# Performance work log

Measured on AMD Instinct MI355X. Metric: run time of the kernel, lower is better.

Reference implementation:

```python
import jax, jax.numpy as jnp
import numpy as np

EPS = 1e-6
BIG = 1e10

# ---- exact Euclidean distance transform (same math as the O(HW*Nfg) brute force,
# factored over rows: d^2(p, fg) = min_{r'} [ (y-r')^2 + min_{x': fg[r',x']} (x-x')^2 ] ----
def edt_2d(fg):  # fg: [H, W] bool -> [H, W] float distance to nearest True pixel
    H, W = fg.shape
    x = jnp.arange(W, dtype=jnp.float32)
    col_d2 = (x[:, None] - x[None, :]) ** 2                              # [W(x), W(x')]
    # colmin[r', x] = min over fg columns x' in row r' of (x-x')^2
    colmin = jnp.min(jnp.where(fg[:, None, :], col_d2[None, :, :], BIG), axis=-1)  # [H, W]
    y = jnp.arange(H, dtype=jnp.float32)
    row_d2 = (y[:, None] - y[None, :]) ** 2                              # [H(y), H(r')]
    d2 = jnp.min(colmin[None, :, :] + row_d2[:, :, None], axis=1)        # [H, W]
    max_dist = jnp.sqrt(jnp.asarray((H - 1) ** 2 + (W - 1) ** 2, jnp.float32))
    has_fg = jnp.any(fg)
    d2_safe = jnp.minimum(d2, (max_dist ** 2))  # only hit when fg empty
    return jnp.where(has_fg, jnp.sqrt(d2_safe), max_dist)


def signed_distance_map(gt):  # gt: [B,1,H,W] float in {0,1}
    gt_bool = gt[:, 0] > 0.5                                             # [B,H,W]
    dist_outside = jax.vmap(edt_2d)(gt_bool)
    dist_inside = jax.vmap(edt_2d)(~gt_bool)
    phi = jnp.where(gt_bool, -dist_inside, dist_outside)                 # [B,H,W]
    return phi[:, None]                                                  # [B,1,H,W]


def boundary_loss(s_theta, g):
    phi = signed_distance_map(g)
    weight = jnp.exp(-jnp.abs(phi) / 10.0)
    return jnp.mean(weight * jnp.abs(phi * s_theta))


def bce_loss(p, t):  # torch nn.BCELoss (log clamped at -100)
    logp = jnp.clip(jnp.log(p), -100.0)
    log1mp = jnp.clip(jnp.log(1.0 - p), -100.0)
    return -jnp.mean(t * logp + (1.0 - t) * log1mp)


def focal_loss(pred, target, alpha=0.25, gamma=2.0):
    pred = jnp.clip(pred, EPS, 1.0 - EPS)
    pt = pred * target + (1.0 - pred) * (1.0 - target)
    alpha_t = alpha * target + (1.0 - alpha) * (1.0 - target)
    return jnp.mean(-alpha_t * (1.0 - pt) ** gamma * jnp.log(pt))


def _gaussian_kernel(ksize=11, sigma=1.5):
    c = (ksize - 1) / 2.0
    g = np.exp(-((np.arange(ksize) - c) ** 2) / (2.0 * sigma ** 2))
    g = g / g.sum()
    k = np.outer(g, g).astype(np.float32)
    return jnp.asarray(k)[None, None]  # [1,1,K,K]

_SSIM_K = _gaussian_kernel()


def _gconv(x):  # x: [B,1,H,W], valid gaussian filter
    return jax.lax.conv_general_dilated(x, _SSIM_K, (1, 1), 'VALID',
                                        dimension_numbers=('NCHW', 'OIHW', 'NCHW'))


def ssim(x, y, data_range=1.0):
    C1 = (0.01 * data_range) ** 2
    C2 = (0.03 * data_range) ** 2
    mu_x, mu_y = _gconv(x), _gconv(y)
    sx = _gconv(x * x) - mu_x ** 2
    sy = _gconv(y * y) - mu_y ** 2
    sxy = _gconv(x * y) - mu_x * mu_y
    num = (2 * mu_x * mu_y + C1) * (2 * sxy + C2)
    den = (mu_x ** 2 + mu_y ** 2 + C1) * (sx + sy + C2)
    return jnp.mean(num / den)


DICE_W = 1.0
BOUNDARY_W = 1.0
FOCAL_W = 1.0
MSE_W = 1.0
FOCAL_ALPHA = 0.25
FOCAL_GAMMA = 2.0


def setup_inputs() -> dict:
    key = jax.random.key(0)
    k1, k2 = jax.random.split(key)
    pred_masks = jax.random.normal(k1, (8, 1, 192, 192), dtype=jnp.float32)
    target_masks = jax.random.randint(k2, (8, 1, 192, 192), 0, 2, dtype=jnp.int32)
    return {"pred_masks": pred_masks, "target_masks": target_masks}


def reference(pred_masks, target_masks):
    t = target_masks.astype(jnp.float32)
    p = jax.nn.sigmoid(pred_masks)
    dice_val = bce_loss(p, t) * DICE_W
    boundary_val = boundary_loss(p, t) * BOUNDARY_W
    focal_val = focal_loss(p, t, FOCAL_ALPHA, FOCAL_GAMMA) * FOCAL_W
    mse_val = ssim(p, t, 1.0) * MSE_W
    return dice_val + boundary_val + focal_val + mse_val
```

## Files before the change

### kernel.cpp

```cpp
#include <hip/hip_runtime.h>
#include <math.h>

#define BATCH 8
#define HH 192
#define WW 192
#define BIGF 1e10f
#define OH (HH - 10)
#define OW (WW - 10)
#define SSIM_ROWS 4
#define SSIM_BPI ((OH + SSIM_ROWS - 1) / SSIM_ROWS)
#define NSSIMBLK (BATCH * SSIM_BPI)
#define NMASKBLK (BATCH * HH)
#define NENVBLK (BATCH * WW)

__device__ __forceinline__ float waveReduceAdd(float v) {
    #pragma unroll
    for (int o = 32; o > 0; o >>= 1) v += __shfl_down(v, o, 64);
    return v;
}

__device__ __forceinline__ int nearestDist(const unsigned long long m0,
                                           const unsigned long long m1,
                                           const unsigned long long m2,
                                           int x) {
    const unsigned long long m[3] = {m0, m1, m2};
    const int wi = x >> 6, b = x & 63;
    int dL = 1 << 29;
    const unsigned long long low = m[wi] << (63 - b);
    if (low) dL = __clzll(low);
    else if (wi >= 1 && m[wi - 1]) dL = b + 1 + __clzll(m[wi - 1]);
    else if (wi == 2 && m[0]) dL = b + 65 + __clzll(m[0]);
    int dR = 1 << 29;
    const unsigned long long high = m[wi] >> b;
    if (high) dR = __ffsll((long long)high) - 1;
    else if (wi <= 1 && m[wi + 1]) dR = (64 - b) + __ffsll((long long)m[wi + 1]) - 1;
    else if (wi == 0 && m[2]) dR = (128 - b) + __ffsll((long long)m[2]) - 1;
    return min(dL, dR);
}

__global__ void prepKernel(const float* __restrict__ pred,
                           const int* __restrict__ tgt,
                           unsigned long long* __restrict__ mask,
                           float* __restrict__ ssimPart) {
    const int x = threadIdx.x;

    if (blockIdx.x >= NSSIMBLK) {
        const int blk = blockIdx.x - NSSIMBLK;
        const int b = blk / HH, r = blk % HH;
        const int t = tgt[(b * HH + r) * WW + x];
        const unsigned long long bal = __ballot(t > 0);
        if ((x & 63) == 0) mask[((size_t)b * 3 + (x >> 6)) * HH + r] = bal;
        return;
    }

    __shared__ __align__(16) float smem[SSIM_ROWS * 5 * WW];
    __shared__ float red1[3];
    const int blk = blockIdx.x;
    const int b = blk / SSIM_BPI;
    const int r0 = (blk % SSIM_BPI) * SSIM_ROWS;

    float g[11];
    {
        float s = 0.0f;
        #pragma unroll
        for (int k = 0; k < 11; ++k) {
            const float d = (float)(k - 5);
            g[k] = __expf(-d * d / 4.5f);
            s += g[k];
        }
        const float inv = 1.0f / s;
        #pragma unroll
        for (int k = 0; k < 11; ++k) g[k] *= inv;
    }

    float acc[SSIM_ROWS][5];
    #pragma unroll
    for (int o = 0; o < SSIM_ROWS; ++o)
        #pragma unroll
        for (int s = 0; s < 5; ++s) acc[o][s] = 0.0f;

    #pragma unroll
    for (int j = 0; j < SSIM_ROWS + 10; ++j) {
        const int row = r0 + j;
        float p = 0.0f, t = 0.0f;
        if (row < HH) {
            const float z = pred[(b * HH + row) * WW + x];
            p = 1.0f / (1.0f + __expf(-z));
            t = (float)tgt[(b * HH + row) * WW + x];
        }
        const float pp = p * p, tt = t * t, pt = p * t;
        #pragma unroll
        for (int o = 0; o < SSIM_ROWS; ++o) {
            const int k = j - o;
            if (k >= 0 && k <= 10) {
                const float gk = g[k];
                acc[o][0] += gk * p;  acc[o][1] += gk * t;
                acc[o][2] += gk * pp; acc[o][3] += gk * tt; acc[o][4] += gk * pt;
            }
        }
    }
    #pragma unroll
    for (int o = 0; o < SSIM_ROWS; ++o)
        #pragma unroll
        for (int s = 0; s < 5; ++s) smem[(o * 5 + s) * WW + x] = acc[o][s];
    __syncthreads();

    float term = 0.0f;
    if (x < OW) {
        #pragma unroll
        for (int o = 0; o < SSIM_ROWS; ++o) {
            if (r0 + o < OH) {
                float mx = 0, my = 0, mxx = 0, myy = 0, mxy = 0;
                #pragma unroll
                for (int k = 0; k < 11; ++k) {
                    mx  += g[k] * smem[(o * 5 + 0) * WW + x + k];
                    my  += g[k] * smem[(o * 5 + 1) * WW + x + k];
                    mxx += g[k] * smem[(o * 5 + 2) * WW + x + k];
                    myy += g[k] * smem[(o * 5 + 3) * WW + x + k];
                    mxy += g[k] * smem[(o * 5 + 4) * WW + x + k];
                }
                const float C1 = 1e-4f, C2 = 9e-4f;
                const float sx = mxx - mx * mx, sy = myy - my * my, sxy = mxy - mx * my;
                const float num = (2.0f * mx * my + C1) * (2.0f * sxy + C2);
                const float den = (mx * mx + my * my + C1) * (sx + sy + C2);
                term += num / den;
            }
        }
    }
    const float s = waveReduceAdd(term);
    const int wid = x >> 6;
    if ((x & 63) == 0) red1[wid] = s;
    __syncthreads();
    if (x == 0) ssimPart[blk] = red1[0] + red1[1] + red1[2];
}

__global__ void envKernel(const float* __restrict__ pred,
                          const unsigned long long* __restrict__ mask,
                          float* __restrict__ envPart) {
    const int b = blockIdx.x / WW, cx = blockIdx.x % WW;
    const int y = threadIdx.x;

    __shared__ __align__(16) float scf[HH];
    __shared__ __align__(16) float scb[HH];
    __shared__ float red[3];

    const unsigned long long m0 = mask[((size_t)b * 3 + 0) * HH + y];
    const unsigned long long m1 = mask[((size_t)b * 3 + 1) * HH + y];
    const unsigned long long m2 = mask[((size_t)b * 3 + 2) * HH + y];
    const float z = pred[(b * HH + y) * WW + cx];

    const int dfg = nearestDist(m0, m1, m2, cx);
    const int dbg = nearestDist(~m0, ~m1, ~m2, cx);
    scf[y] = (dfg >= WW) ? BIGF : (float)(dfg * dfg);
    scb[y] = (dbg >= WW) ? BIGF : (float)(dbg * dbg);
    const unsigned long long fw = (cx < 64) ? m0 : (cx < 128) ? m1 : m2;
    const float tf = (float)((fw >> (cx & 63)) & 1ull);
    __syncthreads();

    float o0 = BIGF, o1 = BIGF, o2 = BIGF, o3 = BIGF;
    float i0 = BIGF, i1 = BIGF, i2 = BIGF, i3 = BIGF;
    const float fy = (float)y;
    #pragma unroll 6
    for (int rp = 0; rp < HH; rp += 4) {
        const float4 vf = *(const float4*)&scf[rp];
        const float4 vb = *(const float4*)&scb[rp];
        const float e0 = fy - (float)rp;
        const float e1 = fy - (float)(rp + 1);
        const float e2 = fy - (float)(rp + 2);
        const float e3 = fy - (float)(rp + 3);
        o0 = fminf(o0, fmaf(e0, e0, vf.x)); i0 = fminf(i0, fmaf(e0, e0, vb.x));
        o1 = fminf(o1, fmaf(e1, e1, vf.y)); i1 = fminf(i1, fmaf(e1, e1, vb.y));
        o2 = fminf(o2, fmaf(e2, e2, vf.z)); i2 = fminf(i2, fmaf(e2, e2, vb.z));
        o3 = fminf(o3, fmaf(e3, e3, vf.w)); i3 = fminf(i3, fmaf(e3, e3, vb.w));
    }
    const float d2o = fminf(fminf(o0, o1), fminf(o2, o3));
    const float d2i = fminf(fminf(i0, i1), fminf(i2, i3));

    const float maxd2 = (float)((HH - 1) * (HH - 1) + (WW - 1) * (WW - 1));
    const float dist_out = sqrtf(fminf(d2o, maxd2));
    const float dist_in  = sqrtf(fminf(d2i, maxd2));

    const float phi = (tf > 0.5f) ? -dist_in : dist_out;
    const float p = 1.0f / (1.0f + __expf(-z));

    const float wgt = __expf(-fabsf(phi) * 0.1f);
    const float bnd = wgt * fabsf(phi * p);
    const float logp   = fmaxf(__logf(p), -100.0f);
    const float log1mp = fmaxf(__logf(1.0f - p), -100.0f);
    const float bce = -(tf * logp + (1.0f - tf) * log1mp);
    const float pc = fminf(fmaxf(p, 1e-6f), 1.0f - 1e-6f);
    const float pt = pc * tf + (1.0f - pc) * (1.0f - tf);
    const float at = 0.25f * tf + 0.75f * (1.0f - tf);
    const float om = 1.0f - pt;
    const float focal = -at * om * om * __logf(pt);

    const float s = waveReduceAdd(bce + focal + bnd);
    const int wid = y >> 6;
    if ((y & 63) == 0) red[wid] = s;
    __syncthreads();
    if (y == 0) envPart[blockIdx.x] = red[0] + red[1] + red[2];
}

__global__ void reduceKernel(const float* __restrict__ envPart,
                             const float* __restrict__ ssimPart,
                             float* __restrict__ out) {
    const int tid = threadIdx.x;
    float s0 = 0, s3 = 0;
    for (int i = tid; i < NENVBLK; i += 1024) s0 += envPart[i];
    for (int i = tid; i < NSSIMBLK; i += 1024) s3 += ssimPart[i];
    s0 = waveReduceAdd(s0);
    s3 = waveReduceAdd(s3);
    __shared__ float red[16][2];
    const int wid = tid >> 6;
    if ((tid & 63) == 0) { red[wid][0] = s0; red[wid][1] = s3; }
    __syncthreads();
    if (tid == 0) {
        float t0 = 0, t3 = 0;
        #pragma unroll
        for (int w = 0; w < 16; ++w) { t0 += red[w][0]; t3 += red[w][1]; }
        const float N1 = (float)(BATCH * HH * WW);
        const float N2 = (float)(BATCH * OH * OW);
        out[0] = t0 / N1 + t3 / N2;
    }
}

extern "C" void kernel_launch(void* const* d_in, const int* in_sizes, int n_in,
                              void* d_out, int out_size, void* d_ws, size_t ws_size,
                              hipStream_t stream) {
    const float* pred = (const float*)d_in[0];
    const int* tgt = (const int*)d_in[1];

    float* ssimPart = (float*)d_ws;
    float* envPart = (float*)((char*)d_ws + 4096);
    unsigned long long* mask = (unsigned long long*)((char*)d_ws + 16384);

    prepKernel<<<NSSIMBLK + NMASKBLK, WW, 0, stream>>>(pred, tgt, mask, ssimPart);
    envKernel<<<NENVBLK, WW, 0, stream>>>(pred, mask, envPart);
    reduceKernel<<<1, 1024, 0, stream>>>(envPart, ssimPart, (float*)d_out);
}
```

Baseline: 23.29 us.

## Split mask-building into its own kernel and co-schedule SSIM with EDT work

Mask ballots move to a small dedicated kernel where each block handles 8 rows, and the SSIM blocks move into the same launch as the distance-transform blocks. The SSIM work now overlaps with the EDT work instead of sitting on the critical path before it. The mask kernel becomes a short dependency stage, and the final reduction block shrinks to 256 threads. In exchange the merged kernel uses the larger SSIM shared-memory allocation for every block, which may lower occupancy for the EDT blocks.

```diff
diff --git a/kernel.cpp b/kernel.cpp
--- a/kernel.cpp
+++ b/kernel.cpp
@@ -10,8 +10,9 @@
 #define SSIM_ROWS 4
 #define SSIM_BPI ((OH + SSIM_ROWS - 1) / SSIM_ROWS)
 #define NSSIMBLK (BATCH * SSIM_BPI)
-#define NMASKBLK (BATCH * HH)
 #define NENVBLK (BATCH * WW)
+#define ROWS_PER_MASKBLK 8
+#define NMASKBLK (BATCH * HH / ROWS_PER_MASKBLK)
 
 __device__ __forceinline__ float waveReduceAdd(float v) {
     #pragma unroll
@@ -38,167 +39,170 @@
     return min(dL, dR);
 }
 
-__global__ void prepKernel(const float* __restrict__ pred,
-                           const int* __restrict__ tgt,
-                           unsigned long long* __restrict__ mask,
-                           float* __restrict__ ssimPart) {
+__global__ void maskKernel(const int* __restrict__ tgt,
+                           unsigned long long* __restrict__ mask) {
     const int x = threadIdx.x;
-
-    if (blockIdx.x >= NSSIMBLK) {
-        const int blk = blockIdx.x - NSSIMBLK;
-        const int b = blk / HH, r = blk % HH;
+    const int b = blockIdx.x / (HH / ROWS_PER_MASKBLK);
+    const int r0 = (blockIdx.x % (HH / ROWS_PER_MASKBLK)) * ROWS_PER_MASKBLK;
+    #pragma unroll
+    for (int j = 0; j < ROWS_PER_MASKBLK; ++j) {
+        const int r = r0 + j;
         const int t = tgt[(b * HH + r) * WW + x];
         const unsigned long long bal = __ballot(t > 0);
         if ((x & 63) == 0) mask[((size_t)b * 3 + (x >> 6)) * HH + r] = bal;
-        return;
     }
-
+}
+
+__global__ void workKernel(const float* __restrict__ pred,
+                           const int* __restrict__ tgt,
+                           const unsigned long long* __restrict__ mask,
+                           float* __restrict__ ssimPart,
+                           float* __restrict__ envPart) {
     __shared__ __align__(16) float smem[SSIM_ROWS * 5 * WW];
-    __shared__ float red1[3];
-    const int blk = blockIdx.x;
-    const int b = blk / SSIM_BPI;
-    const int r0 = (blk % SSIM_BPI) * SSIM_ROWS;
-
-    float g[11];
-    {
-        float s = 0.0f;
-        #pragma unroll
-        for (int k = 0; k < 11; ++k) {
-            const float d = (float)(k - 5);
-            g[k] = __expf(-d * d / 4.5f);
-            s += g[k];
-        }
-        const float inv = 1.0f / s;
-        #pragma unroll
-        for (int k = 0; k < 11; ++k) g[k] *= inv;
+    __shared__ float red[3];
+    const int x = threadIdx.x;
+    const int wid = x >> 6;
+
+    if (blockIdx.x < NSSIMBLK) {
+        const int blk = blockIdx.x;
+        const int b = blk / SSIM_BPI;
+        const int r0 = (blk % SSIM_BPI) * SSIM_ROWS;
+
+        float g[11];
+        {
+            float s = 0.0f;
+            #pragma unroll
+            for (int k = 0; k < 11; ++k) {
+                const float d = (float)(k - 5);
+                g[k] = __expf(-d * d / 4.5f);
+                s += g[k];
+            }
+            const float inv = 1.0f / s;
+            #pragma unroll
+            for (int k = 0; k < 11; ++k) g[k] *= inv;
+        }
+
+        float acc[SSIM_ROWS][5];
+        #pragma unroll
+        for (int o = 0; o < SSIM_ROWS; ++o)
+            #pragma unroll
+            for (int s = 0; s < 5; ++s) acc[o][s] = 0.0f;
+
+        #pragma unroll
+        for (int j = 0; j < SSIM_ROWS + 10; ++j) {
+            const int row = r0 + j;
+            float p = 0.0f, t = 0.0f;
+            if (row < HH) {
+                const float z = pred[(b * HH + row) * WW + x];
+                p = 1.0f / (1.0f + __expf(-z));
+                t = (float)tgt[(b * HH + row) * WW + x];
+            }
+            const float pp = p * p, tt = t * t, pt = p * t;
+            #pragma unroll
+            for (int o = 0; o < SSIM_ROWS; ++o) {
+                const int k = j - o;
+                if (k >= 0 && k <= 10) {
+                    const float gk = g[k];
+                    acc[o][0] += gk * p;  acc[o][1] += gk * t;
+                    acc[o][2] += gk * pp; acc[o][3] += gk * tt; acc[o][4] += gk * pt;
+                }
+            }
+        }
+        #pragma unroll
+        for (int o = 0; o < SSIM_ROWS; ++o)
+            #pragma unroll
+            for (int s = 0; s < 5; ++s) smem[(o * 5 + s) * WW + x] = acc[o][s];
+        __syncthreads();
+
+        float term = 0.0f;
+        if (x < OW) {
+            #pragma unroll
+            for (int o = 0; o < SSIM_ROWS; ++o) {
+                if (r0 + o < OH) {
+                    float mx = 0, my = 0, mxx = 0, myy = 0, mxy = 0;
+                    #pragma unroll
+                    for (int k = 0; k < 11; ++k) {
+                        mx  += g[k] * smem[(o * 5 + 0) * WW + x + k];
+                        my  += g[k] * smem[(o * 5 + 1) * WW + x + k];
+                        mxx += g[k] * smem[(o * 5 + 2) * WW + x + k];
+                        myy += g[k] * smem[(o * 5 + 3) * WW + x + k];
+                        mxy += g[k] * smem[(o * 5 + 4) * WW + x + k];
+                    }
+                    const float C1 = 1e-4f, C2 = 9e-4f;
+                    const float sx = mxx - mx * mx, sy = myy - my * my, sxy = mxy - mx * my;
+                    const float num = (2.0f * mx * my + C1) * (2.0f * sxy + C2);
+                    const float den = (mx * mx + my * my + C1) * (sx + sy + C2);
+                    term += num / den;
+                }
+            }
+        }
+        const float s = waveReduceAdd(term);
+        if ((x & 63) == 0) red[wid] = s;
+        __syncthreads();
+        if (x == 0) ssimPart[blk] = red[0] + red[1] + red[2];
+    } else {
+        const int ebid = blockIdx.x - NSSIMBLK;
+        const int b = ebid / WW, cx = ebid % WW;
+        const int y = x;
+
+        float* scf = smem;
+        float* scb = smem + HH;
+
+        const unsigned long long m0 = mask[((size_t)b * 3 + 0) * HH + y];
+        const unsigned long long m1 = mask[((size_t)b * 3 + 1) * HH + y];
+        const unsigned long long m2 = mask[((size_t)b * 3 + 2) * HH + y];
+        const float z = pred[(b * HH + y) * WW + cx];
+
+        const int dfg = nearestDist(m0, m1, m2, cx);
+        const int dbg = nearestDist(~m0, ~m1, ~m2, cx);
+        scf[y] = (dfg >= WW) ? BIGF : (float)(dfg * dfg);
+        scb[y] = (dbg >= WW) ? BIGF : (float)(dbg * dbg);
+        const unsigned long long fw = (cx < 64) ? m0 : (cx < 128) ? m1 : m2;
+        const float tf = (float)((fw >> (cx & 63)) & 1ull);
+        __syncthreads();
+
+        float o0 = BIGF, o1 = BIGF, o2 = BIGF, o3 = BIGF;
+        float i0 = BIGF, i1 = BIGF, i2 = BIGF, i3 = BIGF;
+        const float fy = (float)y;
+        #pragma unroll 6
+        for (int rp = 0; rp < HH; rp += 4) {
+            const float4 vf = *(const float4*)&scf[rp];
+            const float4 vb = *(const float4*)&scb[rp];
+            const float e0 = fy - (float)rp;
+            const float e1 = fy - (float)(rp + 1);
+            const float e2 = fy - (float)(rp + 2);
+            const float e3 = fy - (float)(rp + 3);
+            o0 = fminf(o0, fmaf(e0, e0, vf.x)); i0 = fminf(i0, fmaf(e0, e0, vb.x));
+            o1 = fminf(o1, fmaf(e1, e1, vf.y)); i1 = fminf(i1, fmaf(e1, e1, vb.y));
+            o2 = fminf(o2, fmaf(e2, e2, vf.z)); i2 = fminf(i2, fmaf(e2, e2, vb.z));
+            o3 = fminf(o3, fmaf(e3, e3, vf.w)); i3 = fminf(i3, fmaf(e3, e3, vb.w));
+        }
+        const float d2o = fminf(fminf(o0, o1), fminf(o2, o3));
+        const float d2i = fminf(fminf(i0, i1), fminf(i2, i3));
+
+        const float maxd2 = (float)((HH - 1) * (HH - 1) + (WW - 1) * (WW - 1));
+        const float dist_out = sqrtf(fminf(d2o, maxd2));
+        const float dist_in  = sqrtf(fminf(d2i, maxd2));
+
+        const float phi = (tf > 0.5f) ? -dist_in : dist_out;
+        const float p = 1.0f / (1.0f + __expf(-z));
+
+        const float wgt = __expf(-fabsf(phi) * 0.1f);
+        const float bnd = wgt * fabsf(phi * p);
+        const float logp   = fmaxf(__logf(p), -100.0f);
+        const float log1mp = fmaxf(__logf(1.0f - p), -100.0f);
+        const float bce = -(tf * logp + (1.0f - tf) * log1mp);
+        const float pc = fminf(fmaxf(p, 1e-6f), 1.0f - 1e-6f);
+        const float pt = pc * tf + (1.0f - pc) * (1.0f - tf);
+        const float at = 0.25f * tf + 0.75f * (1.0f - tf);
+        const float om = 1.0f - pt;
+        const float focal = -at * om * om * __logf(pt);
+
+        const float s = waveReduceAdd(bce + focal + bnd);
+        if ((x & 63) == 0) red[wid] = s;
+        __syncthreads();
+        if (x == 0) envPart[ebid] = red[0] + red[1] + red[2];
     }
-
-    float acc[SSIM_ROWS][5];
-    #pragma unroll
-    for (int o = 0; o < SSIM_ROWS; ++o)
-        #pragma unroll
-        for (int s = 0; s < 5; ++s) acc[o][s] = 0.0f;
-
-    #pragma unroll
-    for (int j = 0; j < SSIM_ROWS + 10; ++j) {
-        const int row = r0 + j;
-        float p = 0.0f, t = 0.0f;
-        if (row < HH) {
-            const float z = pred[(b * HH + row) * WW + x];
-            p = 1.0f / (1.0f + __expf(-z));
-            t = (float)tgt[(b * HH + row) * WW + x];
-        }
-        const float pp = p * p, tt = t * t, pt = p * t;
-        #pragma unroll
-        for (int o = 0; o < SSIM_ROWS; ++o) {
-            const int k = j - o;
-            if (k >= 0 && k <= 10) {
-                const float gk = g[k];
-                acc[o][0] += gk * p;  acc[o][1] += gk * t;
-                acc[o][2] += gk * pp; acc[o][3] += gk * tt; acc[o][4] += gk * pt;
-            }
-        }
-    }
-    #pragma unroll
-    for (int o = 0; o < SSIM_ROWS; ++o)
-        #pragma unroll
-        for (int s = 0; s < 5; ++s) smem[(o * 5 + s) * WW + x] = acc[o][s];
-    __syncthreads();
-
-    float term = 0.0f;
-    if (x < OW) {
-        #pragma unroll
-        for (int o = 0; o < SSIM_ROWS; ++o) {
-            if (r0 + o < OH) {
-                float mx = 0, my = 0, mxx = 0, myy = 0, mxy = 0;
-                #pragma unroll
-                for (int k = 0; k < 11; ++k) {
-                    mx  += g[k] * smem[(o * 5 + 0) * WW + x + k];
-                    my  += g[k] * smem[(o * 5 + 1) * WW + x + k];
-                    mxx += g[k] * smem[(o * 5 + 2) * WW + x + k];
-                    myy += g[k] * smem[(o * 5 + 3) * WW + x + k];
-                    mxy += g[k] * smem[(o * 5 + 4) * WW + x + k];
-                }
-                const float C1 = 1e-4f, C2 = 9e-4f;
-                const float sx = mxx - mx * mx, sy = myy - my * my, sxy = mxy - mx * my;
-                const float num = (2.0f * mx * my + C1) * (2.0f * sxy + C2);
-                const float den = (mx * mx + my * my + C1) * (sx + sy + C2);
-                term += num / den;
-            }
-        }
-    }
-    const float s = waveReduceAdd(term);
-    const int wid = x >> 6;
-    if ((x & 63) == 0) red1[wid] = s;
-    __syncthreads();
-    if (x == 0) ssimPart[blk] = red1[0] + red1[1] + red1[2];
-}
-
-__global__ void envKernel(const float* __restrict__ pred,
-                          const unsigned long long* __restrict__ mask,
-                          float* __restrict__ envPart) {
-    const int b = blockIdx.x / WW, cx = blockIdx.x % WW;
-    const int y = threadIdx.x;
-
-    __shared__ __align__(16) float scf[HH];
-    __shared__ __align__(16) float scb[HH];
-    __shared__ float red[3];
-
-    const unsigned long long m0 = mask[((size_t)b * 3 + 0) * HH + y];
-    const unsigned long long m1 = mask[((size_t)b * 3 + 1) * HH + y];
-    const unsigned long long m2 = mask[((size_t)b * 3 + 2) * HH + y];
-    const float z = pred[(b * HH + y) * WW + cx];
-
-    const int dfg = nearestDist(m0, m1, m2, cx);
-    const int dbg = nearestDist(~m0, ~m1, ~m2, cx);
-    scf[y] = (dfg >= WW) ? BIGF : (float)(dfg * dfg);
-    scb[y] = (dbg >= WW) ? BIGF : (float)(dbg * dbg);
-    const unsigned long long fw = (cx < 64) ? m0 : (cx < 128) ? m1 : m2;
-    const float tf = (float)((fw >> (cx & 63)) & 1ull);
-    __syncthreads();
-
-    float o0 = BIGF, o1 = BIGF, o2 = BIGF, o3 = BIGF;
-    float i0 = BIGF, i1 = BIGF, i2 = BIGF, i3 = BIGF;
-    const float fy = (float)y;
-    #pragma unroll 6
-    for (int rp = 0; rp < HH; rp += 4) {
-        const float4 vf = *(const float4*)&scf[rp];
-        const float4 vb = *(const float4*)&scb[rp];
-        const float e0 = fy - (float)rp;
-        const float e1 = fy - (float)(rp + 1);
-        const float e2 = fy - (float)(rp + 2);
-        const float e3 = fy - (float)(rp + 3);
-        o0 = fminf(o0, fmaf(e0, e0, vf.x)); i0 = fminf(i0, fmaf(e0, e0, vb.x));
-        o1 = fminf(o1, fmaf(e1, e1, vf.y)); i1 = fminf(i1, fmaf(e1, e1, vb.y));
-        o2 = fminf(o2, fmaf(e2, e2, vf.z)); i2 = fminf(i2, fmaf(e2, e2, vb.z));
-        o3 = fminf(o3, fmaf(e3, e3, vf.w)); i3 = fminf(i3, fmaf(e3, e3, vb.w));
-    }
-    const float d2o = fminf(fminf(o0, o1), fminf(o2, o3));
-    const float d2i = fminf(fminf(i0, i1), fminf(i2, i3));
-
-    const float maxd2 = (float)((HH - 1) * (HH - 1) + (WW - 1) * (WW - 1));
-    const float dist_out = sqrtf(fminf(d2o, maxd2));
-    const float dist_in  = sqrtf(fminf(d2i, maxd2));
-
-    const float phi = (tf > 0.5f) ? -dist_in : dist_out;
-    const float p = 1.0f / (1.0f + __expf(-z));
-
-    const float wgt = __expf(-fabsf(phi) * 0.1f);
-    const float bnd = wgt * fabsf(phi * p);
-    const float logp   = fmaxf(__logf(p), -100.0f);
-    const float log1mp = fmaxf(__logf(1.0f - p), -100.0f);
-    const float bce = -(tf * logp + (1.0f - tf) * log1mp);
-    const float pc = fminf(fmaxf(p, 1e-6f), 1.0f - 1e-6f);
-    const float pt = pc * tf + (1.0f - pc) * (1.0f - tf);
-    const float at = 0.25f * tf + 0.75f * (1.0f - tf);
-    const float om = 1.0f - pt;
-    const float focal = -at * om * om * __logf(pt);
-
-    const float s = waveReduceAdd(bce + focal + bnd);
-    const int wid = y >> 6;
-    if ((y & 63) == 0) red[wid] = s;
-    __syncthreads();
-    if (y == 0) envPart[blockIdx.x] = red[0] + red[1] + red[2];
 }
 
 __global__ void reduceKernel(const float* __restrict__ envPart,
@@ -206,18 +210,18 @@
                              float* __restrict__ out) {
     const int tid = threadIdx.x;
     float s0 = 0, s3 = 0;
-    for (int i = tid; i < NENVBLK; i += 1024) s0 += envPart[i];
-    for (int i = tid; i < NSSIMBLK; i += 1024) s3 += ssimPart[i];
+    for (int i = tid; i < NENVBLK; i += 256) s0 += envPart[i];
+    for (int i = tid; i < NSSIMBLK; i += 256) s3 += ssimPart[i];
     s0 = waveReduceAdd(s0);
     s3 = waveReduceAdd(s3);
-    __shared__ float red[16][2];
+    __shared__ float red[4][2];
     const int wid = tid >> 6;
     if ((tid & 63) == 0) { red[wid][0] = s0; red[wid][1] = s3; }
     __syncthreads();
     if (tid == 0) {
         float t0 = 0, t3 = 0;
         #pragma unroll
-        for (int w = 0; w < 16; ++w) { t0 += red[w][0]; t3 += red[w][1]; }
+        for (int w = 0; w < 4; ++w) { t0 += red[w][0]; t3 += red[w][1]; }
         const float N1 = (float)(BATCH * HH * WW);
         const float N2 = (float)(BATCH * OH * OW);
         out[0] = t0 / N1 + t3 / N2;
@@ -234,7 +238,7 @@
     float* envPart = (float*)((char*)d_ws + 4096);
     unsigned long long* mask = (unsigned long long*)((char*)d_ws + 16384);
 
-    prepKernel<<<NSSIMBLK + NMASKBLK, WW, 0, stream>>>(pred, tgt, mask, ssimPart);
-    envKernel<<<NENVBLK, WW, 0, stream>>>(pred, mask, envPart);
-    reduceKernel<<<1, 1024, 0, stream>>>(envPart, ssimPart, (float*)d_out);
-}
+    maskKernel<<<NMASKBLK, WW, 0, stream>>>(tgt, mask);
+    workKernel<<<NSSIMBLK + NENVBLK, WW, 0, stream>>>(pred, tgt, mask, ssimPart, envPart);
+    reduceKernel<<<1, 256, 0, stream>>>(envPart, ssimPart, (float*)d_out);
+}
```

After: 25.05 us. 7.6% more time.
